# Kernel tuning notes

Measured on AMD Instinct MI355X. Metric: run time of the kernel, lower is better.

The kernel has to match this reference:

```python
import jax, jax.numpy as jnp
import numpy as np

REDUCTION = 10.0
EPSILON = 1e-07


def setup_inputs() -> dict:
    key = jax.random.key(0)
    B, P, F = 64, 30720, 32          # events, points per event, features
    N = B * P                        # 1,966,080 total points
    k1, k2, k3 = jax.random.split(key, 3)
    x = jax.random.normal(k1, (N, F), dtype=jnp.float32)
    # random score generated by the layer internally; hoisted here for determinism
    score = jax.random.uniform(k2, (N, 1), dtype=jnp.float32)
    is_track = (jax.random.uniform(k3, (N, 1)) < 0.05).astype(jnp.int32)
    row_splits = (jnp.arange(B + 1, dtype=jnp.int32) * P)
    return {"x": x, "score": score, "is_track": is_track, "row_splits": row_splits}


def reference(x, score, is_track, row_splits):
    N, F = x.shape
    B = row_splits.shape[0] - 1
    # tracks always survive: score forced to 0
    score = jnp.where(is_track.astype(bool), jnp.float32(0.0), score)  # [N,1]
    s = score[:, 0]
    # segment id of each point from row_splits (ragged structure)
    seg = jnp.searchsorted(row_splits, jnp.arange(N, dtype=row_splits.dtype), side='right') - 1
    # per-event min score, then global max -> adaptive threshold guaranteeing >=1 point/event
    min_event_score = jax.ops.segment_min(s, seg, num_segments=B)
    highest_min = jnp.max(min_event_score)
    inv_r = jnp.float32(1.0 / REDUCTION)
    threshold = jnp.where(highest_min < inv_r, inv_r, highest_min + jnp.float32(EPSILON))
    mask = s <= threshold                                              # [N] keep-mask
    # new row_splits from per-event selected counts
    counts = jax.ops.segment_sum(mask.astype(jnp.int32), seg, num_segments=B)
    new_rs = jnp.concatenate([jnp.zeros((1,), jnp.int32), jnp.cumsum(counts)])
    # stable compaction: selected indices first, in original order (== boolean_mask order)
    order = jnp.argsort(jnp.logical_not(mask), stable=True)            # [N]
    n_sel = new_rs[-1]
    valid = jnp.arange(N) < n_sel                                      # [N]
    x_sel = jnp.where(valid[:, None], x[order], jnp.float32(0.0))      # [N,F], rows >= n_sel are padding
    indices_selected = jnp.where(valid, order, -1).astype(jnp.int32)[:, None]  # [N,1], -1 = padding
    old_size = jnp.int32(N)
    return x_sel, new_rs, old_size, indices_selected, n_sel
```

## Files before the change

kernel.cpp:

```cpp
#include <hip/hip_runtime.h>
#include <stdint.h>

#define BS 256
#define CPB 4

typedef unsigned long long u64;

__global__ __launch_bounds__(BS)
void k_segmin(const float* __restrict__ score, const int* __restrict__ track,
              const int* __restrict__ rs, int B, int SPS,
              float* __restrict__ part_min) {
    int b = blockIdx.x;
    int s = b / SPS, j = b - s * SPS;
    int r0 = rs[s], r1 = rs[s + 1];
    int len = r1 - r0;
    int per = (len + SPS - 1) / SPS;
    int a = r0 + j * per;
    int e = min(r1, a + per);
    float m = INFINITY;
    for (int i = a + (int)threadIdx.x; i < e; i += BS)
        m = fminf(m, track[i] ? 0.0f : score[i]);
    for (int d = 32; d > 0; d >>= 1) m = fminf(m, __shfl_down(m, d));
    __shared__ float wmin[BS / 64];
    if ((threadIdx.x & 63) == 0) wmin[threadIdx.x >> 6] = m;
    __syncthreads();
    if (threadIdx.x == 0) {
        float mm = wmin[0];
        for (int k = 1; k < BS / 64; ++k) mm = fminf(mm, wmin[k]);
        part_min[b] = mm;
    }
}

__global__ __launch_bounds__(BS)
void k_count(const float* __restrict__ score, const int* __restrict__ track,
             const float* __restrict__ part_min, int N, int B, int SPS,
             u64* __restrict__ gmask, int* __restrict__ cnts) {
    const int b = blockIdx.x, tid = threadIdx.x;
    const int w = tid >> 6, lane = tid & 63;
    __shared__ float shT;
    __shared__ u64 smask[CPB * 4];

    if (tid < 64) {
        float m = -INFINITY;
        for (int s = tid; s < B; s += 64) {
            float mn = INFINITY;
            for (int j = 0; j < SPS; ++j) mn = fminf(mn, part_min[s * SPS + j]);
            m = fmaxf(m, mn);
        }
        for (int d = 32; d > 0; d >>= 1) m = fmaxf(m, __shfl_xor(m, d));
        if (tid == 0) shT = (m < 0.1f) ? 0.1f : (m + 1e-7f);
    }
    __syncthreads();
    const float T = shT;

    const long Rb = (long)b * CPB * BS;
    for (int c = 0; c < CPB; ++c) {
        long i = Rb + (long)c * BS + tid;
        bool pred = (i < N) && ((track[i] ? 0.0f : score[i]) <= T);
        u64 bal = __ballot(pred);
        if (lane == 0) smask[c * 4 + w] = bal;
    }
    __syncthreads();
    if (tid < CPB * 4) gmask[(long)b * CPB * 4 + tid] = smask[tid];
    if (tid == 0) {
        int c = 0;
        for (int k = 0; k < CPB * 4; ++k) c += __popcll(smask[k]);
        cnts[b] = c;
    }
}

__global__ __launch_bounds__(BS)
void k_main(const float* __restrict__ x, const int* __restrict__ rsp,
            const u64* __restrict__ gmask, const int* __restrict__ cnts,
            int N, int B, int F, int G2,
            float* __restrict__ out_x, float* __restrict__ out_rs,
            float* __restrict__ out_old, float* __restrict__ out_idx,
            float* __restrict__ out_nsel) {
    const int b = blockIdx.x, tid = threadIdx.x;
    const int w = tid >> 6, lane = tid & 63;
    const int RPB = CPB * BS;
    const int Rb = b * RPB;
    const int Lact = min(RPB, N - Rb);

    __shared__ u64 smask[CPB * 4];
    __shared__ int chunkcnt[CPB];
    __shared__ int rows[CPB * BS];
    __shared__ int shBase, shTot;

    if (tid < CPB * 4) smask[tid] = gmask[(long)b * CPB * 4 + tid];

    if (tid < 64) {
        int pre = 0, tot = 0;
        for (int k = tid; k < G2; k += 64) {
            int c = cnts[k];
            tot += c;
            pre += (k < b) ? c : 0;
        }
        for (int d = 32; d > 0; d >>= 1) {
            pre += __shfl_down(pre, d);
            tot += __shfl_down(tot, d);
        }
        if (tid == 0) { shBase = pre; shTot = tot; }
    }
    __syncthreads();
    if (tid < CPB) {
        const u64* mw = &smask[tid * 4];
        chunkcnt[tid] = __popcll(mw[0]) + __popcll(mw[1]) + __popcll(mw[2]) + __popcll(mw[3]);
    }
    __syncthreads();
    const int myBase = shBase, total = shTot;

    if (b == 0 && tid == 0) { out_nsel[0] = (float)total; out_old[0] = (float)N; }

    int bcnt = 0;
    {
        int basec = 0;
        for (int c = 0; c < CPB; ++c) {
            u64 mybal = smask[c * 4 + w];
            int wb = 0;
            for (int k = 0; k < w; ++k) wb += __popcll(smask[c * 4 + k]);
            if ((mybal >> (unsigned)lane) & 1ULL) {
                int rank = basec + wb + __popcll(mybal & ((1ULL << (unsigned)lane) - 1ULL));
                int row = Rb + c * BS + tid;
                rows[rank] = row;
                out_idx[(long)myBase + rank] = (float)row;
            }
            basec += chunkcnt[c];
        }
        bcnt = basec;
    }
    __syncthreads();

    const int Fv = F >> 2;
    const bool vec = ((F & 3) == 0) && (Fv > 0) && (BS % Fv == 0);
    const float4* x4 = (const float4*)x;
    float4* out4 = (float4*)out_x;

    if (vec) {
        int r0 = tid / Fv, cc = tid - r0 * Fv, rstep = BS / Fv;
        for (int r = r0; r < bcnt; r += rstep)
            out4[((long)myBase + r) * Fv + cc] = x4[(long)rows[r] * Fv + cc];
    } else {
        for (int e = tid; e < bcnt * F; e += BS) {
            int r = e / F, cc = e - r * F;
            out_x[((long)myBase + r) * F + cc] = x[(long)rows[r] * F + cc];
        }
    }

    int unsel = Lact - bcnt;
    long Unext = (long)(Rb + Lact) - (long)(myBase + bcnt);
    long zr0 = (long)N - Unext;
    if (vec) {
        float4 z = make_float4(0.0f, 0.0f, 0.0f, 0.0f);
        long e0 = zr0 * Fv, ecnt = (long)unsel * Fv;
        for (long e = tid; e < ecnt; e += BS) out4[e0 + e] = z;
    } else {
        long e0 = zr0 * (long)F, ecnt = (long)unsel * F;
        for (long e = tid; e < ecnt; e += BS) out_x[e0 + e] = 0.0f;
    }
    for (int t = tid; t < unsel; t += BS) out_idx[zr0 + t] = -1.0f;

    for (int s = tid; s <= B; s += BS) {
        int pos = rsp[s];
        if (pos >= Rb && pos < Rb + Lact) {
            int rel = pos - Rb;
            int nw = rel >> 6, rem = rel & 63;
            int cnt = 0;
            for (int k = 0; k < nw; ++k) cnt += __popcll(smask[k]);
            if (rem) cnt += __popcll(smask[nw] & ((1ULL << (unsigned)rem) - 1ULL));
            out_rs[s] = (float)(myBase + cnt);
        } else if (b == G2 - 1 && pos >= N) {
            out_rs[s] = (float)total;
        }
    }
}

extern "C" void kernel_launch(void* const* d_in, const int* in_sizes, int n_in,
                              void* d_out, int out_size, void* d_ws, size_t ws_size,
                              hipStream_t stream) {
    const float* x     = (const float*)d_in[0];
    const float* score = (const float*)d_in[1];
    const int*   track = (const int*)d_in[2];
    const int*   rs    = (const int*)d_in[3];

    int N = in_sizes[1];
    int F = in_sizes[0] / N;
    int B = in_sizes[3] - 1;

    int nchunks = (N + BS - 1) / BS;
    int G2 = (nchunks + CPB - 1) / CPB;

    int SPS = B > 0 ? (1024 / B) : 1;
    if (SPS < 1) SPS = 1;
    if (SPS > 64) SPS = 64;
    int G1 = B * SPS;

    float* part_min = (float*)d_ws;
    int*   cnts     = (int*)(part_min + G1);
    u64*   gmask    = (u64*)(((uintptr_t)(cnts + G2) + 15) & ~(uintptr_t)15);

    float* out      = (float*)d_out;
    long off_rs   = (long)N * F;
    long off_old  = off_rs + (B + 1);
    long off_idx  = off_old + 1;
    long off_nsel = off_idx + N;

    float* out_x    = out;
    float* out_rs   = out + off_rs;
    float* out_old  = out + off_old;
    float* out_idx  = out + off_idx;
    float* out_nsel = out + off_nsel;

    k_segmin<<<G1, BS, 0, stream>>>(score, track, rs, B, SPS, part_min);
    k_count<<<G2, BS, 0, stream>>>(score, track, part_min, N, B, SPS, gmask, cnts);
    k_main<<<G2, BS, 0, stream>>>(x, rs, gmask, cnts, N, B, F, G2,
                                  out_x, out_rs, out_old, out_idx, out_nsel);
}
```

Measured before the change: 83.52 us.

## Split padding zero-fill into separate kernel and use nontemporal loads/stores

Moves zero-filling of the unselected tail of out_x and out_idx out of the per-block compaction kernel into a new grid-stride kernel. It uses a global total that k_count accumulates atomically, and k_segmin resets that total at the start. All streaming loads and stores of x, score, track and the outputs now use nontemporal builtins to avoid polluting the cache. The intent is to balance the write work evenly across blocks and cut cache thrashing, at the cost of an extra kernel launch and an atomic per block.

```diff
diff --git a/kernel.cpp b/kernel.cpp
--- a/kernel.cpp
+++ b/kernel.cpp
@@ -5,12 +5,20 @@
 #define CPB 4
 
 typedef unsigned long long u64;
+typedef float f32x4 __attribute__((ext_vector_type(4)));
+
+__device__ __forceinline__ void nt_store4(f32x4* p, f32x4 v) { __builtin_nontemporal_store(v, p); }
+__device__ __forceinline__ f32x4 nt_load4(const f32x4* p) { return __builtin_nontemporal_load(p); }
+__device__ __forceinline__ void nt_storef(float* p, float v) { __builtin_nontemporal_store(v, p); }
+__device__ __forceinline__ float nt_loadf(const float* p) { return __builtin_nontemporal_load(p); }
+__device__ __forceinline__ int nt_loadi(const int* p) { return __builtin_nontemporal_load(p); }
 
 __global__ __launch_bounds__(BS)
 void k_segmin(const float* __restrict__ score, const int* __restrict__ track,
               const int* __restrict__ rs, int B, int SPS,
-              float* __restrict__ part_min) {
+              float* __restrict__ part_min, int* __restrict__ ws_total) {
     int b = blockIdx.x;
+    if (b == 0 && threadIdx.x == 0) *ws_total = 0;
     int s = b / SPS, j = b - s * SPS;
     int r0 = rs[s], r1 = rs[s + 1];
     int len = r1 - r0;
@@ -34,7 +42,8 @@
 __global__ __launch_bounds__(BS)
 void k_count(const float* __restrict__ score, const int* __restrict__ track,
              const float* __restrict__ part_min, int N, int B, int SPS,
-             u64* __restrict__ gmask, int* __restrict__ cnts) {
+             u64* __restrict__ gmask, int* __restrict__ cnts,
+             int* __restrict__ ws_total) {
     const int b = blockIdx.x, tid = threadIdx.x;
     const int w = tid >> 6, lane = tid & 63;
     __shared__ float shT;
@@ -56,7 +65,7 @@
     const long Rb = (long)b * CPB * BS;
     for (int c = 0; c < CPB; ++c) {
         long i = Rb + (long)c * BS + tid;
-        bool pred = (i < N) && ((track[i] ? 0.0f : score[i]) <= T);
+        bool pred = (i < N) && ((nt_loadi(&track[i]) ? 0.0f : nt_loadf(&score[i])) <= T);
         u64 bal = __ballot(pred);
         if (lane == 0) smask[c * 4 + w] = bal;
     }
@@ -66,11 +75,12 @@
         int c = 0;
         for (int k = 0; k < CPB * 4; ++k) c += __popcll(smask[k]);
         cnts[b] = c;
-    }
-}
-
-__global__ __launch_bounds__(BS)
-void k_main(const float* __restrict__ x, const int* __restrict__ rsp,
+        atomicAdd(ws_total, c);
+    }
+}
+
+__global__ __launch_bounds__(BS)
+void k_copy(const float* __restrict__ x, const int* __restrict__ rsp,
             const u64* __restrict__ gmask, const int* __restrict__ cnts,
             int N, int B, int F, int G2,
             float* __restrict__ out_x, float* __restrict__ out_rs,
@@ -123,7 +133,7 @@
                 int rank = basec + wb + __popcll(mybal & ((1ULL << (unsigned)lane) - 1ULL));
                 int row = Rb + c * BS + tid;
                 rows[rank] = row;
-                out_idx[(long)myBase + rank] = (float)row;
+                nt_storef(&out_idx[(long)myBase + rank], (float)row);
             }
             basec += chunkcnt[c];
         }
@@ -133,32 +143,22 @@
 
     const int Fv = F >> 2;
     const bool vec = ((F & 3) == 0) && (Fv > 0) && (BS % Fv == 0);
-    const float4* x4 = (const float4*)x;
-    float4* out4 = (float4*)out_x;
+    const f32x4* x4 = (const f32x4*)x;
+    f32x4* out4 = (f32x4*)out_x;
 
     if (vec) {
         int r0 = tid / Fv, cc = tid - r0 * Fv, rstep = BS / Fv;
-        for (int r = r0; r < bcnt; r += rstep)
-            out4[((long)myBase + r) * Fv + cc] = x4[(long)rows[r] * Fv + cc];
+        for (int r = r0; r < bcnt; r += rstep) {
+            f32x4 v = nt_load4(&x4[(long)rows[r] * Fv + cc]);
+            nt_store4(&out4[((long)myBase + r) * Fv + cc], v);
+        }
     } else {
         for (int e = tid; e < bcnt * F; e += BS) {
             int r = e / F, cc = e - r * F;
-            out_x[((long)myBase + r) * F + cc] = x[(long)rows[r] * F + cc];
-        }
-    }
-
-    int unsel = Lact - bcnt;
-    long Unext = (long)(Rb + Lact) - (long)(myBase + bcnt);
-    long zr0 = (long)N - Unext;
-    if (vec) {
-        float4 z = make_float4(0.0f, 0.0f, 0.0f, 0.0f);
-        long e0 = zr0 * Fv, ecnt = (long)unsel * Fv;
-        for (long e = tid; e < ecnt; e += BS) out4[e0 + e] = z;
-    } else {
-        long e0 = zr0 * (long)F, ecnt = (long)unsel * F;
-        for (long e = tid; e < ecnt; e += BS) out_x[e0 + e] = 0.0f;
-    }
-    for (int t = tid; t < unsel; t += BS) out_idx[zr0 + t] = -1.0f;
+            nt_storef(&out_x[((long)myBase + r) * F + cc],
+                      nt_loadf(&x[(long)rows[r] * F + cc]));
+        }
+    }
 
     for (int s = tid; s <= B; s += BS) {
         int pos = rsp[s];
@@ -175,6 +175,25 @@
     }
 }
 
+__global__ __launch_bounds__(BS)
+void k_zero(const int* __restrict__ ws_total, int N, int F,
+            float* __restrict__ out_x, float* __restrict__ out_idx) {
+    const int total = *ws_total;
+    const long stride = (long)gridDim.x * BS;
+    const long off = (long)blockIdx.x * BS + threadIdx.x;
+    if ((F & 3) == 0) {
+        const int Fv = F >> 2;
+        f32x4* out4 = (f32x4*)out_x;
+        f32x4 z = (f32x4)(0.0f);
+        long e0 = (long)total * Fv, e1 = (long)N * Fv;
+        for (long e = e0 + off; e < e1; e += stride) nt_store4(&out4[e], z);
+    } else {
+        long e0 = (long)total * F, e1 = (long)N * F;
+        for (long e = e0 + off; e < e1; e += stride) nt_storef(&out_x[e], 0.0f);
+    }
+    for (long t = total + off; t < N; t += stride) nt_storef(&out_idx[t], -1.0f);
+}
+
 extern "C" void kernel_launch(void* const* d_in, const int* in_sizes, int n_in,
                               void* d_out, int out_size, void* d_ws, size_t ws_size,
                               hipStream_t stream) {
@@ -196,7 +215,8 @@
     int G1 = B * SPS;
 
     float* part_min = (float*)d_ws;
-    int*   cnts     = (int*)(part_min + G1);
+    int*   ws_total = (int*)(part_min + G1);
+    int*   cnts     = ws_total + 1;
     u64*   gmask    = (u64*)(((uintptr_t)(cnts + G2) + 15) & ~(uintptr_t)15);
 
     float* out      = (float*)d_out;
@@ -211,8 +231,9 @@
     float* out_idx  = out + off_idx;
     float* out_nsel = out + off_nsel;
 
-    k_segmin<<<G1, BS, 0, stream>>>(score, track, rs, B, SPS, part_min);
-    k_count<<<G2, BS, 0, stream>>>(score, track, part_min, N, B, SPS, gmask, cnts);
-    k_main<<<G2, BS, 0, stream>>>(x, rs, gmask, cnts, N, B, F, G2,
+    k_segmin<<<G1, BS, 0, stream>>>(score, track, rs, B, SPS, part_min, ws_total);
+    k_count<<<G2, BS, 0, stream>>>(score, track, part_min, N, B, SPS, gmask, cnts, ws_total);
+    k_copy<<<G2, BS, 0, stream>>>(x, rs, gmask, cnts, N, B, F, G2,
                                   out_x, out_rs, out_old, out_idx, out_nsel);
-}
+    k_zero<<<2048, BS, 0, stream>>>(ws_total, N, F, out_x, out_idx);
+}
```

Measured after the change: 108.9 us. 1.3x slower.

## Switch compaction from source-block scatter to destination-block gather

Applied to the files above, without the earlier changes.

Each write block now owns a contiguous range of output rows. It finds the source chunk whose prefix count covers its start, walks the mask words with a wave-level scan to collect the source row indices, then gathers x rows into its own output range and fills the remaining rows with zeros. Output writes become fully contiguous per block, and the scattered zero and index writes that the old per-source-block layout produced go away. Row splits are moved to extra blocks that each compute one prefix count. The cost is a serial mask walk per block and a scan of all chunk counts for each block.

```diff
diff --git a/kernel.cpp b/kernel.cpp
--- a/kernel.cpp
+++ b/kernel.cpp
@@ -3,8 +3,11 @@
 
 #define BS 256
 #define CPB 4
+#define RPB (CPB * BS)
+#define WPC (RPB / 64)
 
 typedef unsigned long long u64;
+typedef float f32x4 __attribute__((ext_vector_type(4)));
 
 __global__ __launch_bounds__(BS)
 void k_segmin(const float* __restrict__ score, const int* __restrict__ track,
@@ -38,7 +41,7 @@
     const int b = blockIdx.x, tid = threadIdx.x;
     const int w = tid >> 6, lane = tid & 63;
     __shared__ float shT;
-    __shared__ u64 smask[CPB * 4];
+    __shared__ u64 smask[WPC];
 
     if (tid < 64) {
         float m = -INFINITY;
@@ -53,7 +56,7 @@
     __syncthreads();
     const float T = shT;
 
-    const long Rb = (long)b * CPB * BS;
+    const long Rb = (long)b * RPB;
     for (int c = 0; c < CPB; ++c) {
         long i = Rb + (long)c * BS + tid;
         bool pred = (i < N) && ((track[i] ? 0.0f : score[i]) <= T);
@@ -61,118 +64,133 @@
         if (lane == 0) smask[c * 4 + w] = bal;
     }
     __syncthreads();
-    if (tid < CPB * 4) gmask[(long)b * CPB * 4 + tid] = smask[tid];
+    if (tid < WPC) gmask[(long)b * WPC + tid] = smask[tid];
     if (tid == 0) {
         int c = 0;
-        for (int k = 0; k < CPB * 4; ++k) c += __popcll(smask[k]);
+        for (int k = 0; k < WPC; ++k) c += __popcll(smask[k]);
         cnts[b] = c;
     }
 }
 
 __global__ __launch_bounds__(BS)
-void k_main(const float* __restrict__ x, const int* __restrict__ rsp,
-            const u64* __restrict__ gmask, const int* __restrict__ cnts,
-            int N, int B, int F, int G2,
-            float* __restrict__ out_x, float* __restrict__ out_rs,
-            float* __restrict__ out_old, float* __restrict__ out_idx,
-            float* __restrict__ out_nsel) {
+void k_write(const float* __restrict__ x, const int* __restrict__ rsp,
+             const u64* __restrict__ gmask, const int* __restrict__ cnts,
+             int N, int B, int F, int G2, int OB,
+             float* __restrict__ out_x, float* __restrict__ out_rs,
+             float* __restrict__ out_old, float* __restrict__ out_idx,
+             float* __restrict__ out_nsel) {
     const int b = blockIdx.x, tid = threadIdx.x;
-    const int w = tid >> 6, lane = tid & 63;
-    const int RPB = CPB * BS;
-    const int Rb = b * RPB;
-    const int Lact = min(RPB, N - Rb);
-
-    __shared__ u64 smask[CPB * 4];
-    __shared__ int chunkcnt[CPB];
-    __shared__ int rows[CPB * BS];
-    __shared__ int shBase, shTot;
-
-    if (tid < CPB * 4) smask[tid] = gmask[(long)b * CPB * 4 + tid];
-
-    if (tid < 64) {
-        int pre = 0, tot = 0;
-        for (int k = tid; k < G2; k += 64) {
-            int c = cnts[k];
-            tot += c;
-            pre += (k < b) ? c : 0;
-        }
-        for (int d = 32; d > 0; d >>= 1) {
-            pre += __shfl_down(pre, d);
-            tot += __shfl_down(tot, d);
-        }
-        if (tid == 0) { shBase = pre; shTot = tot; }
-    }
-    __syncthreads();
-    if (tid < CPB) {
-        const u64* mw = &smask[tid * 4];
-        chunkcnt[tid] = __popcll(mw[0]) + __popcll(mw[1]) + __popcll(mw[2]) + __popcll(mw[3]);
-    }
-    __syncthreads();
-    const int myBase = shBase, total = shTot;
+    const int lane = tid & 63, wv = tid >> 6;
+    const int Wall = G2 * WPC;
+
+    __shared__ int srcRows[RPB];
+    __shared__ int shCb0, shBase0, shTot;
+    __shared__ long wsum[BS / 64];
+
+    if (b >= OB) {
+        int sb = b - OB;
+        int pos = rsp[sb];
+        int cbP = pos / RPB;
+        int within = pos - cbP * RPB;
+        long sum = 0;
+        for (int k = tid; k < cbP; k += BS) sum += cnts[k];
+        if (tid == 0) {
+            int fw = within >> 6, rem = within & 63;
+            int wb = cbP * WPC;
+            for (int k2 = 0; k2 < fw; ++k2) sum += __popcll(gmask[wb + k2]);
+            if (rem) sum += __popcll(gmask[wb + fw] & ((1ull << rem) - 1ull));
+        }
+        for (int d = 32; d > 0; d >>= 1) sum += __shfl_down(sum, d);
+        if (lane == 0) wsum[wv] = sum;
+        __syncthreads();
+        if (tid == 0) {
+            long s = 0;
+            for (int k = 0; k < BS / 64; ++k) s += wsum[k];
+            out_rs[sb] = (float)s;
+        }
+        return;
+    }
+
+    const int D0 = b * RPB;
+    const int D1 = min(N, D0 + RPB);
+
+    if (wv == 0) {
+        int S = (G2 + 63) / 64;
+        int lo = min(G2, lane * S), hi = min(G2, lane * S + S);
+        int ssum = 0;
+        for (int k = lo; k < hi; ++k) ssum += cnts[k];
+        int incl = ssum;
+        for (int d = 1; d < 64; d <<= 1) { int t = __shfl_up(incl, d); if (lane >= d) incl += t; }
+        int sbase = incl - ssum;
+        u64 m = __ballot(sbase <= D0);
+        int H = 63 - __clzll(m);
+        if (lane == H) {
+            int run = sbase; int cb = lo;
+            for (; cb < hi; ++cb) { int c = cnts[cb]; if (run + c > D0) break; run += c; }
+            shCb0 = cb; shBase0 = run;
+        }
+        if (lane == 63) shTot = incl;
+    }
+    __syncthreads();
+    const int total = shTot;
+    const int selCnt = max(0, min(D1, total) - D0);
 
     if (b == 0 && tid == 0) { out_nsel[0] = (float)total; out_old[0] = (float)N; }
 
-    int bcnt = 0;
-    {
-        int basec = 0;
-        for (int c = 0; c < CPB; ++c) {
-            u64 mybal = smask[c * 4 + w];
-            int wb = 0;
-            for (int k = 0; k < w; ++k) wb += __popcll(smask[c * 4 + k]);
-            if ((mybal >> (unsigned)lane) & 1ULL) {
-                int rank = basec + wb + __popcll(mybal & ((1ULL << (unsigned)lane) - 1ULL));
-                int row = Rb + c * BS + tid;
-                rows[rank] = row;
-                out_idx[(long)myBase + rank] = (float)row;
+    if (wv == 0 && selCnt > 0) {
+        int wBase = shCb0 * WPC;
+        long acc = shBase0;
+        while (true) {
+            int wi = wBase + lane;
+            u64 word = (wi < Wall) ? gmask[wi] : 0ull;
+            int p = __popcll(word);
+            int incl = p;
+            for (int d = 1; d < 64; d <<= 1) { int t = __shfl_up(incl, d); if (lane >= d) incl += t; }
+            long wstart = acc + (incl - p);
+            if (word && (wstart + p > (long)D0) && (wstart < (long)D0 + selCnt)) {
+                u64 w2 = word; int j = 0;
+                while (w2) {
+                    int bit = __ffsll((long long)w2) - 1;
+                    long slot = wstart + j - D0;
+                    if (slot >= 0 && slot < selCnt) srcRows[slot] = wi * 64 + bit;
+                    w2 &= w2 - 1; ++j;
+                }
             }
-            basec += chunkcnt[c];
-        }
-        bcnt = basec;
-    }
-    __syncthreads();
-
+            long wtot = __shfl(incl, 63);
+            acc += wtot;
+            wBase += 64;
+            if (acc >= (long)D0 + selCnt || wBase >= Wall) break;
+        }
+    }
+    __syncthreads();
+
+    const int nrows = D1 - D0;
     const int Fv = F >> 2;
-    const bool vec = ((F & 3) == 0) && (Fv > 0) && (BS % Fv == 0);
-    const float4* x4 = (const float4*)x;
-    float4* out4 = (float4*)out_x;
-
-    if (vec) {
-        int r0 = tid / Fv, cc = tid - r0 * Fv, rstep = BS / Fv;
-        for (int r = r0; r < bcnt; r += rstep)
-            out4[((long)myBase + r) * Fv + cc] = x4[(long)rows[r] * Fv + cc];
+    if ((F & 3) == 0 && Fv > 0 && (BS % Fv) == 0) {
+        const f32x4* x4 = (const f32x4*)x;
+        f32x4* o4 = (f32x4*)out_x + (long)D0 * Fv;
+        const int rstep = BS / Fv;
+        int r0 = tid / Fv, cc = tid - r0 * Fv;
+        int r = r0;
+        for (; r < selCnt; r += rstep)
+            o4[(long)r * Fv + cc] = x4[(long)srcRows[r] * Fv + cc];
+        f32x4 z = (f32x4)(0.0f);
+        for (; r < nrows; r += rstep)
+            o4[(long)r * Fv + cc] = z;
     } else {
-        for (int e = tid; e < bcnt * F; e += BS) {
+        float* o = out_x + (long)D0 * F;
+        int selE = selCnt * F, allE = nrows * F;
+        int e = tid;
+        for (; e < selE; e += BS) {
             int r = e / F, cc = e - r * F;
-            out_x[((long)myBase + r) * F + cc] = x[(long)rows[r] * F + cc];
-        }
-    }
-
-    int unsel = Lact - bcnt;
-    long Unext = (long)(Rb + Lact) - (long)(myBase + bcnt);
-    long zr0 = (long)N - Unext;
-    if (vec) {
-        float4 z = make_float4(0.0f, 0.0f, 0.0f, 0.0f);
-        long e0 = zr0 * Fv, ecnt = (long)unsel * Fv;
-        for (long e = tid; e < ecnt; e += BS) out4[e0 + e] = z;
-    } else {
-        long e0 = zr0 * (long)F, ecnt = (long)unsel * F;
-        for (long e = tid; e < ecnt; e += BS) out_x[e0 + e] = 0.0f;
-    }
-    for (int t = tid; t < unsel; t += BS) out_idx[zr0 + t] = -1.0f;
-
-    for (int s = tid; s <= B; s += BS) {
-        int pos = rsp[s];
-        if (pos >= Rb && pos < Rb + Lact) {
-            int rel = pos - Rb;
-            int nw = rel >> 6, rem = rel & 63;
-            int cnt = 0;
-            for (int k = 0; k < nw; ++k) cnt += __popcll(smask[k]);
-            if (rem) cnt += __popcll(smask[nw] & ((1ULL << (unsigned)rem) - 1ULL));
-            out_rs[s] = (float)(myBase + cnt);
-        } else if (b == G2 - 1 && pos >= N) {
-            out_rs[s] = (float)total;
-        }
-    }
+            o[e] = x[(long)srcRows[r] * F + cc];
+        }
+        for (; e < allE; e += BS) o[e] = 0.0f;
+    }
+    float* oi = out_idx + D0;
+    int t2 = tid;
+    for (; t2 < selCnt; t2 += BS) oi[t2] = (float)srcRows[t2];
+    for (; t2 < nrows; t2 += BS) oi[t2] = -1.0f;
 }
 
 extern "C" void kernel_launch(void* const* d_in, const int* in_sizes, int n_in,
@@ -187,8 +205,8 @@
     int F = in_sizes[0] / N;
     int B = in_sizes[3] - 1;
 
-    int nchunks = (N + BS - 1) / BS;
-    int G2 = (nchunks + CPB - 1) / CPB;
+    int G2 = (N + RPB - 1) / RPB;
+    int OB = G2;
 
     int SPS = B > 0 ? (1024 / B) : 1;
     if (SPS < 1) SPS = 1;
@@ -213,6 +231,6 @@
 
     k_segmin<<<G1, BS, 0, stream>>>(score, track, rs, B, SPS, part_min);
     k_count<<<G2, BS, 0, stream>>>(score, track, part_min, N, B, SPS, gmask, cnts);
-    k_main<<<G2, BS, 0, stream>>>(x, rs, gmask, cnts, N, B, F, G2,
-                                  out_x, out_rs, out_old, out_idx, out_nsel);
-}
+    k_write<<<OB + B + 1, BS, 0, stream>>>(x, rs, gmask, cnts, N, B, F, G2, OB,
+                                           out_x, out_rs, out_old, out_idx, out_nsel);
+}
```

After: 95.54 us. 1.14x slower.

## Prefetch gathered rows before zero-fill and parallelize prefix count in k_main

Applied to the files above, without the earlier changes.

The gather loop in k_main is restructured so each thread issues up to eight independent float4 row loads up front, writes the zero padding and -1 indices while those loads are in flight, then stores the gathered rows. The block-prefix computation over per-block counts now uses all four waves instead of one, and the per-warp rank base is computed from register popcounts, dropping one __syncthreads. This is meant to raise memory-level parallelism and shorten the serial setup before the copy, at the cost of more registers per thread.

```diff
diff --git a/kernel.cpp b/kernel.cpp
--- a/kernel.cpp
+++ b/kernel.cpp
@@ -3,8 +3,11 @@
 
 #define BS 256
 #define CPB 4
+#define NW 16
+#define PF 8
 
 typedef unsigned long long u64;
+typedef float f32x4 __attribute__((ext_vector_type(4)));
 
 __global__ __launch_bounds__(BS)
 void k_segmin(const float* __restrict__ score, const int* __restrict__ track,
@@ -38,7 +41,7 @@
     const int b = blockIdx.x, tid = threadIdx.x;
     const int w = tid >> 6, lane = tid & 63;
     __shared__ float shT;
-    __shared__ u64 smask[CPB * 4];
+    __shared__ u64 smask[NW];
 
     if (tid < 64) {
         float m = -INFINITY;
@@ -61,10 +64,10 @@
         if (lane == 0) smask[c * 4 + w] = bal;
     }
     __syncthreads();
-    if (tid < CPB * 4) gmask[(long)b * CPB * 4 + tid] = smask[tid];
+    if (tid < NW) gmask[(long)b * NW + tid] = smask[tid];
     if (tid == 0) {
         int c = 0;
-        for (int k = 0; k < CPB * 4; ++k) c += __popcll(smask[k]);
+        for (int k = 0; k < NW; ++k) c += __popcll(smask[k]);
         cnts[b] = c;
     }
 }
@@ -82,92 +85,116 @@
     const int Rb = b * RPB;
     const int Lact = min(RPB, N - Rb);
 
-    __shared__ u64 smask[CPB * 4];
-    __shared__ int chunkcnt[CPB];
-    __shared__ int rows[CPB * BS];
-    __shared__ int shBase, shTot;
-
-    if (tid < CPB * 4) smask[tid] = gmask[(long)b * CPB * 4 + tid];
-
-    if (tid < 64) {
-        int pre = 0, tot = 0;
-        for (int k = tid; k < G2; k += 64) {
-            int c = cnts[k];
-            tot += c;
-            pre += (k < b) ? c : 0;
-        }
-        for (int d = 32; d > 0; d >>= 1) {
-            pre += __shfl_down(pre, d);
-            tot += __shfl_down(tot, d);
-        }
-        if (tid == 0) { shBase = pre; shTot = tot; }
-    }
-    __syncthreads();
-    if (tid < CPB) {
-        const u64* mw = &smask[tid * 4];
-        chunkcnt[tid] = __popcll(mw[0]) + __popcll(mw[1]) + __popcll(mw[2]) + __popcll(mw[3]);
-    }
-    __syncthreads();
-    const int myBase = shBase, total = shTot;
+    __shared__ u64 smask[NW];
+    __shared__ int rows[RPB];
+    __shared__ int shPre[BS / 64], shTot4[BS / 64];
+
+    if (tid < NW) smask[tid] = gmask[(long)b * NW + tid];
+
+    int pre = 0, tot = 0;
+    for (int k = tid; k < G2; k += BS) {
+        int c = cnts[k];
+        tot += c;
+        pre += (k < b) ? c : 0;
+    }
+    for (int d = 32; d > 0; d >>= 1) {
+        pre += __shfl_down(pre, d);
+        tot += __shfl_down(tot, d);
+    }
+    if (lane == 0) { shPre[w] = pre; shTot4[w] = tot; }
+    __syncthreads();
+    int myBase = 0, total = 0;
+#pragma unroll
+    for (int k = 0; k < BS / 64; ++k) { myBase += shPre[k]; total += shTot4[k]; }
 
     if (b == 0 && tid == 0) { out_nsel[0] = (float)total; out_old[0] = (float)N; }
 
+    int p[NW];
+#pragma unroll
+    for (int j = 0; j < NW; ++j) p[j] = __popcll(smask[j]);
     int bcnt = 0;
-    {
-        int basec = 0;
-        for (int c = 0; c < CPB; ++c) {
-            u64 mybal = smask[c * 4 + w];
-            int wb = 0;
-            for (int k = 0; k < w; ++k) wb += __popcll(smask[c * 4 + k]);
-            if ((mybal >> (unsigned)lane) & 1ULL) {
-                int rank = basec + wb + __popcll(mybal & ((1ULL << (unsigned)lane) - 1ULL));
-                int row = Rb + c * BS + tid;
-                rows[rank] = row;
-                out_idx[(long)myBase + rank] = (float)row;
-            }
-            basec += chunkcnt[c];
-        }
-        bcnt = basec;
+#pragma unroll
+    for (int j = 0; j < NW; ++j) bcnt += p[j];
+
+#pragma unroll
+    for (int c = 0; c < CPB; ++c) {
+        u64 mybal = smask[c * 4 + w];
+        if ((mybal >> (unsigned)lane) & 1ULL) {
+            int basew = 0;
+#pragma unroll
+            for (int j = 0; j < NW; ++j) basew += (j < c * 4 + w) ? p[j] : 0;
+            int rank = basew + __popcll(mybal & ((1ULL << (unsigned)lane) - 1ULL));
+            int row = Rb + c * BS + tid;
+            rows[rank] = row;
+            out_idx[(long)myBase + rank] = (float)row;
+        }
     }
     __syncthreads();
 
     const int Fv = F >> 2;
     const bool vec = ((F & 3) == 0) && (Fv > 0) && (BS % Fv == 0);
-    const float4* x4 = (const float4*)x;
-    float4* out4 = (float4*)out_x;
+
+    const int unsel = Lact - bcnt;
+    const long Unext = (long)(Rb + Lact) - (long)(myBase + bcnt);
+    const long zr0 = (long)N - Unext;
 
     if (vec) {
-        int r0 = tid / Fv, cc = tid - r0 * Fv, rstep = BS / Fv;
-        for (int r = r0; r < bcnt; r += rstep)
-            out4[((long)myBase + r) * Fv + cc] = x4[(long)rows[r] * Fv + cc];
+        const f32x4* x4 = (const f32x4*)x;
+        f32x4* o4 = (f32x4*)out_x;
+        const int rstep = BS / Fv;
+        const int r0 = tid / Fv, cc = tid - (tid / Fv) * Fv;
+
+        f32x4 v0, v1, v2, v3, v4, v5, v6, v7;
+        const int q0 = r0,             q1 = r0 + rstep,     q2 = r0 + 2 * rstep,
+                  q3 = r0 + 3 * rstep, q4 = r0 + 4 * rstep, q5 = r0 + 5 * rstep,
+                  q6 = r0 + 6 * rstep, q7 = r0 + 7 * rstep;
+        if (q0 < bcnt) v0 = x4[(long)rows[q0] * Fv + cc];
+        if (q1 < bcnt) v1 = x4[(long)rows[q1] * Fv + cc];
+        if (q2 < bcnt) v2 = x4[(long)rows[q2] * Fv + cc];
+        if (q3 < bcnt) v3 = x4[(long)rows[q3] * Fv + cc];
+        if (q4 < bcnt) v4 = x4[(long)rows[q4] * Fv + cc];
+        if (q5 < bcnt) v5 = x4[(long)rows[q5] * Fv + cc];
+        if (q6 < bcnt) v6 = x4[(long)rows[q6] * Fv + cc];
+        if (q7 < bcnt) v7 = x4[(long)rows[q7] * Fv + cc];
+
+        {
+            f32x4 z = (f32x4)(0.0f);
+            f32x4* zb = o4 + zr0 * Fv;
+            const int ecnt = unsel * Fv;
+            for (int e = tid; e < ecnt; e += BS) zb[e] = z;
+        }
+        for (int t = tid; t < unsel; t += BS) out_idx[zr0 + t] = -1.0f;
+
+        f32x4* ob = o4 + (long)myBase * Fv;
+        if (q0 < bcnt) ob[(long)q0 * Fv + cc] = v0;
+        if (q1 < bcnt) ob[(long)q1 * Fv + cc] = v1;
+        if (q2 < bcnt) ob[(long)q2 * Fv + cc] = v2;
+        if (q3 < bcnt) ob[(long)q3 * Fv + cc] = v3;
+        if (q4 < bcnt) ob[(long)q4 * Fv + cc] = v4;
+        if (q5 < bcnt) ob[(long)q5 * Fv + cc] = v5;
+        if (q6 < bcnt) ob[(long)q6 * Fv + cc] = v6;
+        if (q7 < bcnt) ob[(long)q7 * Fv + cc] = v7;
+
+        for (int r = r0 + PF * rstep; r < bcnt; r += rstep)
+            ob[(long)r * Fv + cc] = x4[(long)rows[r] * Fv + cc];
     } else {
         for (int e = tid; e < bcnt * F; e += BS) {
-            int r = e / F, cc = e - r * F;
-            out_x[((long)myBase + r) * F + cc] = x[(long)rows[r] * F + cc];
-        }
-    }
-
-    int unsel = Lact - bcnt;
-    long Unext = (long)(Rb + Lact) - (long)(myBase + bcnt);
-    long zr0 = (long)N - Unext;
-    if (vec) {
-        float4 z = make_float4(0.0f, 0.0f, 0.0f, 0.0f);
-        long e0 = zr0 * Fv, ecnt = (long)unsel * Fv;
-        for (long e = tid; e < ecnt; e += BS) out4[e0 + e] = z;
-    } else {
+            int r = e / F, cc2 = e - r * F;
+            out_x[((long)myBase + r) * F + cc2] = x[(long)rows[r] * F + cc2];
+        }
         long e0 = zr0 * (long)F, ecnt = (long)unsel * F;
         for (long e = tid; e < ecnt; e += BS) out_x[e0 + e] = 0.0f;
-    }
-    for (int t = tid; t < unsel; t += BS) out_idx[zr0 + t] = -1.0f;
+        for (int t = tid; t < unsel; t += BS) out_idx[zr0 + t] = -1.0f;
+    }
 
     for (int s = tid; s <= B; s += BS) {
         int pos = rsp[s];
         if (pos >= Rb && pos < Rb + Lact) {
             int rel = pos - Rb;
-            int nw = rel >> 6, rem = rel & 63;
+            int nw2 = rel >> 6, rem = rel & 63;
             int cnt = 0;
-            for (int k = 0; k < nw; ++k) cnt += __popcll(smask[k]);
-            if (rem) cnt += __popcll(smask[nw] & ((1ULL << (unsigned)rem) - 1ULL));
+            for (int k = 0; k < nw2; ++k) cnt += __popcll(smask[k]);
+            if (rem) cnt += __popcll(smask[nw2] & ((1ULL << (unsigned)rem) - 1ULL));
             out_rs[s] = (float)(myBase + cnt);
         } else if (b == G2 - 1 && pos >= N) {
             out_rs[s] = (float)total;
```

After: 78.45 us. 6.1% less time.
